# Optimization experiments

Measured on AMD Instinct MI355X. Metric: run time of the kernel, lower is better.

## Reference

```python
import jax, jax.numpy as jnp
import numpy as np

N, F = 16384, 32
H1, H2, D1, D2 = 64, 64, 32, 1


def setup_inputs() -> dict:
    key = jax.random.key(0)
    ks = jax.random.split(key, 10)
    x = jax.random.normal(ks[0], (N, F), dtype=jnp.float32)
    # pre-normalized adjacency (GCNConv expects D^-1/2 A D^-1/2); mimic with uniform/N
    a = jax.random.uniform(ks[1], (N, N), dtype=jnp.float32) / N
    # glorot-ish scaled params
    W1 = jax.random.normal(ks[2], (F, H1), dtype=jnp.float32) * (1.0 / np.sqrt(F))
    b1 = jnp.zeros((H1,), dtype=jnp.float32)
    W2 = jax.random.normal(ks[3], (H1, H2), dtype=jnp.float32) * (1.0 / np.sqrt(H1))
    b2 = jnp.zeros((H2,), dtype=jnp.float32)
    Wd1 = jax.random.normal(ks[4], (H2, D1), dtype=jnp.float32) * (1.0 / np.sqrt(H2))
    bd1 = jnp.zeros((D1,), dtype=jnp.float32)
    Wd2 = jax.random.normal(ks[5], (D1, D2), dtype=jnp.float32) * (1.0 / np.sqrt(D1))
    bd2 = jnp.zeros((D2,), dtype=jnp.float32)
    return {"x": x, "a": a, "W1": W1, "b1": b1, "W2": W2, "b2": b2,
            "Wd1": Wd1, "bd1": bd1, "Wd2": Wd2, "bd2": bd2}


def reference(x, a, W1, b1, W2, b2, Wd1, bd1, Wd2, bd2):
    # GCNConv: relu(a @ (x @ W) + b)   (a is pre-normalized)
    g1 = jax.nn.relu(a @ (x @ W1) + b1)   # [N, 64]
    g2 = jax.nn.relu(a @ (g1 @ W2) + b2)  # [N, 64]
    d3 = jax.nn.relu(g2 @ Wd1 + bd1)      # [N, 32]
    return d3 @ Wd2 + bd2                 # [N, 1]
```

## Files before the change

### kernel.cpp

```cpp
#include <hip/hip_runtime.h>
#include <hip/hip_bf16.h>


typedef __bf16 bf16x8 __attribute__((ext_vector_type(8)));
typedef float  f32x16 __attribute__((ext_vector_type(16)));
typedef float  f32x4v __attribute__((ext_vector_type(4)));
typedef int    i32x4  __attribute__((ext_vector_type(4)));

#define NNODE 16384
#define KDIM  16384
#define HCOL  64

__device__ inline i32x4 pack8(f32x4v a, f32x4v b){
  bf16x8 t;
  t[0]=(__bf16)a[0]; t[1]=(__bf16)a[1]; t[2]=(__bf16)a[2]; t[3]=(__bf16)a[3];
  t[4]=(__bf16)b[0]; t[5]=(__bf16)b[1]; t[6]=(__bf16)b[2]; t[7]=(__bf16)b[3];
  return __builtin_bit_cast(i32x4, t);
}
#define BC(x) __builtin_bit_cast(bf16x8, x)

__global__ __launch_bounds__(256, 1) void gcn_layer_kernel(
    const float* __restrict__ A,
    const __bf16* __restrict__ Ht,
    float* __restrict__ gP)
{
  __shared__ i32x4 sA[4*2*512];
  __shared__ i32x4 sH[2*512];

  const int tid  = threadIdx.x;
  const int lane = tid & 63;
  const int wid  = tid >> 6;
  const int bid  = blockIdx.x;
  const int kq   = bid & 3;
  const int row0 = (bid >> 2) * 256 + wid * 64;

  const int rA0  = lane >> 3;
  const int ccA  = lane & 7;
  const int swzA = ccA ^ rA0;
  const int r    = lane & 31;
  const int hsub = lane >> 5;
  const int xs   = r & 7;

  const int hrow = tid >> 2;
  const int cc2  = (tid & 3) * 2;

  const size_t k0 = (size_t)kq * 4096;

  f32x4v ra[16]; i32x4 rh[2];

  const float* pA0 = A + (size_t)(row0 + rA0) * KDIM + k0 + (size_t)ccA*8;
  const i32x4* pH0 = (const i32x4*)(Ht + (size_t)hrow * KDIM + k0) + cc2;

  auto stage_load = [&](int t){
    const float* pA = pA0 + (size_t)t*64;
    #pragma unroll
    for (int pi=0; pi<8; ++pi){
      const float* p = pA + (size_t)pi*8*KDIM;
      ra[2*pi]   = __builtin_nontemporal_load((const f32x4v*)p);
      ra[2*pi+1] = __builtin_nontemporal_load((const f32x4v*)(p+4));
    }
    rh[0] = pH0[(size_t)t*8];
    rh[1] = pH0[(size_t)t*8 + 1];
  };

  auto stage_write = [&](int buf){
    i32x4* dA = &sA[(wid*2+buf)*512];
    #pragma unroll
    for (int pi=0; pi<8; ++pi)
      dA[(rA0 + pi*8)*8 + swzA] = pack8(ra[2*pi], ra[2*pi+1]);
    i32x4* dH = &sH[buf*512 + hrow*8];
    dH[cc2 ^ (hrow & 7)]       = rh[0];
    dH[(cc2+1) ^ (hrow & 7)]   = rh[1];
  };

  f32x16 acc00 = {}, acc01 = {}, acc10 = {}, acc11 = {};

  auto compute = [&](int buf){
    const i32x4* bA = &sA[(wid*2+buf)*512];
    const i32x4* bH = &sH[buf*512];
    #pragma unroll
    for (int kk=0; kk<4; ++kk){
      int c = (kk*2 + hsub) ^ xs;
      bf16x8 a0 = BC(bA[r*8 + c]);
      bf16x8 a1 = BC(bA[(r+32)*8 + c]);
      bf16x8 b0 = BC(bH[r*8 + c]);
      bf16x8 b1 = BC(bH[(r+32)*8 + c]);
      acc00 = __builtin_amdgcn_mfma_f32_32x32x16_bf16(a0, b0, acc00, 0,0,0);
      acc01 = __builtin_amdgcn_mfma_f32_32x32x16_bf16(a0, b1, acc01, 0,0,0);
      acc10 = __builtin_amdgcn_mfma_f32_32x32x16_bf16(a1, b0, acc10, 0,0,0);
      acc11 = __builtin_amdgcn_mfma_f32_32x32x16_bf16(a1, b1, acc11, 0,0,0);
    }
  };

  stage_load(0);
  stage_write(0);
  stage_load(1);
  __syncthreads();
  #pragma unroll 1
  for (int t=0; t<63; ++t){
    int nx = t+2; if (nx > 63) nx = 63;
    compute(t&1);
    __syncthreads();
    stage_write((t+1)&1);
    stage_load(nx);
    __syncthreads();
  }
  compute(1);

  float* out = gP + ((size_t)kq * NNODE + row0) * HCOL;
  #pragma unroll
  for (int j=0; j<16; ++j){
    int rr = (j&3) + 8*(j>>2) + 4*hsub;
    out[(size_t)(rr     )*HCOL + r]      = acc00[j];
    out[(size_t)(rr     )*HCOL + 32 + r] = acc01[j];
    out[(size_t)(rr + 32)*HCOL + r]      = acc10[j];
    out[(size_t)(rr + 32)*HCOL + 32 + r] = acc11[j];
  }
}

__global__ __launch_bounds__(256) void reduce_kernel(
    const float* __restrict__ gP,
    const float* __restrict__ bias,
    float* __restrict__ g)
{
  const size_t i = (size_t)blockIdx.x * 256 + threadIdx.x;
  const f32x4v* p = (const f32x4v*)gP;
  f32x4v s = p[i];
  s += p[i +  262144];
  s += p[i +  524288];
  s += p[i +  786432];
  f32x4v b = *(const f32x4v*)(bias + (i & 15) * 4);
  f32x4v o;
  o[0] = fmaxf(s[0] + b[0], 0.f);
  o[1] = fmaxf(s[1] + b[1], 0.f);
  o[2] = fmaxf(s[2] + b[2], 0.f);
  o[3] = fmaxf(s[3] + b[3], 0.f);
  ((f32x4v*)g)[i] = o;
}

template<int F>
__global__ __launch_bounds__(128) void proj_T_kernel(
    const float* __restrict__ in,
    const float* __restrict__ W,
    __bf16* __restrict__ out)
{
  constexpr int FP = F + 4;
  __shared__ float sWt[64*FP];
  __shared__ short sOut[64*136];

  int tid = threadIdx.x;
  for (int e = tid; e < 64*F; e += 128){
    int h = e / F, j = e - h*F;
    sWt[h*FP + j] = W[j*64 + h];
  }
  __syncthreads();

  const size_t n = (size_t)blockIdx.x*128 + tid;
  float rowv[F];
  #pragma unroll
  for (int j=0; j<F; j+=4){
    f32x4v v = *(const f32x4v*)(in + n*F + j);
    rowv[j]=v[0]; rowv[j+1]=v[1]; rowv[j+2]=v[2]; rowv[j+3]=v[3];
  }
  #pragma unroll
  for (int h=0; h<64; ++h){
    float s = 0.f;
    #pragma unroll
    for (int j=0; j<F; j+=4){
      f32x4v w = *(const f32x4v*)&sWt[h*FP + j];
      s += rowv[j]*w[0] + rowv[j+1]*w[1] + rowv[j+2]*w[2] + rowv[j+3]*w[3];
    }
    sOut[h*136 + tid] = __builtin_bit_cast(short, (__bf16)s);
  }
  __syncthreads();

  const size_t n0 = (size_t)blockIdx.x*128;
  #pragma unroll
  for (int pi=0; pi<8; ++pi){
    int p = pi*128 + tid;
    int h = p >> 4, cc = p & 15;
    i32x4 v = *(const i32x4*)&sOut[h*136 + cc*8];
    *(i32x4*)(out + (size_t)h*NNODE + n0 + cc*8) = v;
  }
}

__global__ __launch_bounds__(256) void tail_kernel(
    const float* __restrict__ g2,
    const float* __restrict__ Wd1,
    const float* __restrict__ bd1,
    const float* __restrict__ Wd2,
    const float* __restrict__ bd2,
    float* __restrict__ outp)
{
  __shared__ float sW[64*32];
  __shared__ float sb1[32], sw2[32];
  int tid = threadIdx.x;
  for (int e=tid; e<2048; e+=256) sW[e] = Wd1[e];
  if (tid < 32){ sb1[tid] = bd1[tid]; sw2[tid] = Wd2[tid]; }
  __syncthreads();

  size_t n = (size_t)blockIdx.x*256 + tid;
  float rv[64];
  #pragma unroll
  for (int j=0;j<64;j+=4){
    f32x4v v = *(const f32x4v*)(g2 + n*64 + j);
    rv[j]=v[0]; rv[j+1]=v[1]; rv[j+2]=v[2]; rv[j+3]=v[3];
  }
  float o = 0.f;
  #pragma unroll
  for (int c=0;c<32;++c){
    float s = sb1[c];
    #pragma unroll
    for (int j=0;j<64;++j) s += rv[j]*sW[j*32 + c];
    o += fmaxf(s, 0.f) * sw2[c];
  }
  outp[n] = o + bd2[0];
}

extern "C" void kernel_launch(void* const* d_in, const int* in_sizes, int n_in,
                              void* d_out, int out_size, void* d_ws, size_t ws_size,
                              hipStream_t stream)
{
  const float* x   = (const float*)d_in[0];
  const float* a   = (const float*)d_in[1];
  const float* W1  = (const float*)d_in[2];
  const float* b1  = (const float*)d_in[3];
  const float* W2  = (const float*)d_in[4];
  const float* b2  = (const float*)d_in[5];
  const float* Wd1 = (const float*)d_in[6];
  const float* bd1 = (const float*)d_in[7];
  const float* Wd2 = (const float*)d_in[8];
  const float* bd2 = (const float*)d_in[9];
  float* outp = (float*)d_out;

  char* ws = (char*)d_ws;
  __bf16* Ht1 = (__bf16*)(ws);
  __bf16* Ht2 = (__bf16*)(ws + (2u<<20));
  float*  g1  = (float*)(ws + (4u<<20));
  float*  g2  = (float*)(ws + (8u<<20));
  float*  gP  = (float*)(ws + (12u<<20));

  proj_T_kernel<32><<<128, 128, 0, stream>>>(x,  W1, Ht1);
  gcn_layer_kernel <<<256, 256, 0, stream>>>(a, Ht1, gP);
  reduce_kernel    <<<1024, 256, 0, stream>>>(gP, b1, g1);
  proj_T_kernel<64><<<128, 128, 0, stream>>>(g1, W2, Ht2);
  gcn_layer_kernel <<<256, 256, 0, stream>>>(a, Ht2, gP);
  reduce_kernel    <<<1024, 256, 0, stream>>>(gP, b2, g2);
  tail_kernel      <<<64, 256, 0, stream>>>(g2, Wd1, bd1, Wd2, bd2, outp);
}
```

Measured before the change: 495.9 us.

## Halve split-K, stream H from global per wave, and drop block barriers

```diff
diff --git a/kernel.cpp b/kernel.cpp
--- a/kernel.cpp
+++ b/kernel.cpp
@@ -19,102 +19,96 @@
 }
 #define BC(x) __builtin_bit_cast(bf16x8, x)
 
-__global__ __launch_bounds__(256, 1) void gcn_layer_kernel(
+__global__ __launch_bounds__(256, 2) void gcn_layer_kernel(
     const float* __restrict__ A,
     const __bf16* __restrict__ Ht,
     float* __restrict__ gP)
 {
   __shared__ i32x4 sA[4*2*512];
-  __shared__ i32x4 sH[2*512];
 
   const int tid  = threadIdx.x;
   const int lane = tid & 63;
   const int wid  = tid >> 6;
   const int bid  = blockIdx.x;
-  const int kq   = bid & 3;
-  const int row0 = (bid >> 2) * 256 + wid * 64;
-
-  const int rA0  = lane >> 3;
-  const int ccA  = lane & 7;
-  const int swzA = ccA ^ rA0;
+  const int kh   = (bid >> 2) & 1;
+  const int rowblk = (bid & 3) | ((bid >> 3) << 2);
+  const int row0 = rowblk * 128 + wid * 32;
+
+  const int srow = lane >> 4;
+  const int scol = lane & 15;
   const int r    = lane & 31;
   const int hsub = lane >> 5;
-  const int xs   = r & 7;
-
-  const int hrow = tid >> 2;
-  const int cc2  = (tid & 3) * 2;
-
-  const size_t k0 = (size_t)kq * 4096;
-
-  f32x4v ra[16]; i32x4 rh[2];
-
-  const float* pA0 = A + (size_t)(row0 + rA0) * KDIM + k0 + (size_t)ccA*8;
-  const i32x4* pH0 = (const i32x4*)(Ht + (size_t)hrow * KDIM + k0) + cc2;
+  const int x15  = r & 15;
+
+  const size_t k0 = (size_t)kh * 8192;
+
+  f32x4v ra[16];
+  i32x4  rb0[8], rb1[8];
+
+  const float*  pA0 = A  + (size_t)(row0 + srow) * KDIM + k0 + (size_t)scol * 8;
+  const __bf16* pB0 = Ht + (size_t)r        * KDIM + k0 + (size_t)hsub * 8;
+  const __bf16* pB1 = pB0 + (size_t)32 * KDIM;
 
   auto stage_load = [&](int t){
-    const float* pA = pA0 + (size_t)t*64;
-    #pragma unroll
-    for (int pi=0; pi<8; ++pi){
-      const float* p = pA + (size_t)pi*8*KDIM;
-      ra[2*pi]   = __builtin_nontemporal_load((const f32x4v*)p);
-      ra[2*pi+1] = __builtin_nontemporal_load((const f32x4v*)(p+4));
-    }
-    rh[0] = pH0[(size_t)t*8];
-    rh[1] = pH0[(size_t)t*8 + 1];
+    const float* p = pA0 + (size_t)t * 128;
+    #pragma unroll
+    for (int gg = 0; gg < 8; ++gg){
+      const float* q = p + (size_t)gg * 4 * KDIM;
+      ra[2*gg]   = __builtin_nontemporal_load((const f32x4v*)q);
+      ra[2*gg+1] = __builtin_nontemporal_load((const f32x4v*)(q + 4));
+    }
   };
 
   auto stage_write = [&](int buf){
-    i32x4* dA = &sA[(wid*2+buf)*512];
-    #pragma unroll
-    for (int pi=0; pi<8; ++pi)
-      dA[(rA0 + pi*8)*8 + swzA] = pack8(ra[2*pi], ra[2*pi+1]);
-    i32x4* dH = &sH[buf*512 + hrow*8];
-    dH[cc2 ^ (hrow & 7)]       = rh[0];
-    dH[(cc2+1) ^ (hrow & 7)]   = rh[1];
-  };
-
-  f32x16 acc00 = {}, acc01 = {}, acc10 = {}, acc11 = {};
-
-  auto compute = [&](int buf){
-    const i32x4* bA = &sA[(wid*2+buf)*512];
-    const i32x4* bH = &sH[buf*512];
-    #pragma unroll
-    for (int kk=0; kk<4; ++kk){
-      int c = (kk*2 + hsub) ^ xs;
-      bf16x8 a0 = BC(bA[r*8 + c]);
-      bf16x8 a1 = BC(bA[(r+32)*8 + c]);
-      bf16x8 b0 = BC(bH[r*8 + c]);
-      bf16x8 b1 = BC(bH[(r+32)*8 + c]);
-      acc00 = __builtin_amdgcn_mfma_f32_32x32x16_bf16(a0, b0, acc00, 0,0,0);
-      acc01 = __builtin_amdgcn_mfma_f32_32x32x16_bf16(a0, b1, acc01, 0,0,0);
-      acc10 = __builtin_amdgcn_mfma_f32_32x32x16_bf16(a1, b0, acc10, 0,0,0);
-      acc11 = __builtin_amdgcn_mfma_f32_32x32x16_bf16(a1, b1, acc11, 0,0,0);
+    i32x4* dA = &sA[(wid*2 + buf) * 512];
+    #pragma unroll
+    for (int gg = 0; gg < 8; ++gg){
+      int row = gg*4 + srow;
+      dA[row*16 + (scol ^ (row & 15))] = pack8(ra[2*gg], ra[2*gg+1]);
+    }
+  };
+
+  auto loadB = [&](int t){
+    const __bf16* q0 = pB0 + (size_t)t * 128;
+    const __bf16* q1 = pB1 + (size_t)t * 128;
+    #pragma unroll
+    for (int kk = 0; kk < 8; ++kk){
+      rb0[kk] = *(const i32x4*)(q0 + kk*16);
+      rb1[kk] = *(const i32x4*)(q1 + kk*16);
+    }
+  };
+
+  f32x16 acc0 = {}, acc1 = {};
+
+  auto compute = [&](int buf, int t){
+    loadB(t);
+    const i32x4* bA = &sA[(wid*2 + buf) * 512];
+    #pragma unroll
+    for (int kk = 0; kk < 8; ++kk){
+      int c = (kk*2 + hsub) ^ x15;
+      bf16x8 a0 = BC(bA[r*16 + c]);
+      acc0 = __builtin_amdgcn_mfma_f32_32x32x16_bf16(a0, BC(rb0[kk]), acc0, 0,0,0);
+      acc1 = __builtin_amdgcn_mfma_f32_32x32x16_bf16(a0, BC(rb1[kk]), acc1, 0,0,0);
     }
   };
 
   stage_load(0);
   stage_write(0);
   stage_load(1);
-  __syncthreads();
   #pragma unroll 1
-  for (int t=0; t<63; ++t){
-    int nx = t+2; if (nx > 63) nx = 63;
-    compute(t&1);
-    __syncthreads();
-    stage_write((t+1)&1);
-    stage_load(nx);
-    __syncthreads();
-  }
-  compute(1);
-
-  float* out = gP + ((size_t)kq * NNODE + row0) * HCOL;
-  #pragma unroll
-  for (int j=0; j<16; ++j){
+  for (int t = 0; t < 63; ++t){
+    compute(t & 1, t);
+    stage_write((t+1) & 1);
+    if (t < 62) stage_load(t + 2);
+  }
+  compute(1, 63);
+
+  float* out = gP + ((size_t)kh * NNODE + row0) * HCOL;
+  #pragma unroll
+  for (int j = 0; j < 16; ++j){
     int rr = (j&3) + 8*(j>>2) + 4*hsub;
-    out[(size_t)(rr     )*HCOL + r]      = acc00[j];
-    out[(size_t)(rr     )*HCOL + 32 + r] = acc01[j];
-    out[(size_t)(rr + 32)*HCOL + r]      = acc10[j];
-    out[(size_t)(rr + 32)*HCOL + 32 + r] = acc11[j];
+    out[(size_t)rr * HCOL + r]      = acc0[j];
+    out[(size_t)rr * HCOL + 32 + r] = acc1[j];
   }
 }
 
@@ -125,10 +119,7 @@
 {
   const size_t i = (size_t)blockIdx.x * 256 + threadIdx.x;
   const f32x4v* p = (const f32x4v*)gP;
-  f32x4v s = p[i];
-  s += p[i +  262144];
-  s += p[i +  524288];
-  s += p[i +  786432];
+  f32x4v s = p[i] + p[i + 262144];
   f32x4v b = *(const f32x4v*)(bias + (i & 15) * 4);
   f32x4v o;
   o[0] = fmaxf(s[0] + b[0], 0.f);
```

New measurement: 605.3 us. 1.22x slower.
